# Optimization experiments

Measured on AMD Instinct MI355X. Metric: run time of the kernel, lower is better.

Reference implementation:

```python
import jax, jax.numpy as jnp
import numpy as np

MARGIN = 0.3


def setup_inputs() -> dict:
    key = jax.random.key(0)
    k1, k2 = jax.random.split(key)
    embeddings = jax.random.normal(k1, (4096, 128), dtype=jnp.float32)
    labels = jax.random.randint(k2, (4096,), 0, 256, dtype=jnp.int64)
    return {"embeddings": embeddings, "labels": labels}


def reference(embeddings, labels):
    # L2-normalize rows (same as F.normalize(p=2, dim=1), eps=1e-12)
    norm = jnp.maximum(jnp.linalg.norm(embeddings, axis=1, keepdims=True), 1e-12)
    e = embeddings / norm
    # cosine distance matrix [N, N]
    dist = 1.0 - e @ e.T

    same = labels[None, :] == labels[:, None]          # [N, N]
    n = labels.shape[0]
    eye = jnp.eye(n, dtype=bool)
    pos_mask = same & ~eye                             # positives excl. self
    neg_mask = ~same

    # dist in [0, 2]; finite sentinels keep max/min well-defined per row
    hardest_pos = jnp.max(jnp.where(pos_mask, dist, -1.0), axis=1)
    hardest_neg = jnp.min(jnp.where(neg_mask, dist, 3.0), axis=1)

    valid = jnp.any(pos_mask, axis=1) & jnp.any(neg_mask, axis=1)
    per_row = jax.nn.relu(hardest_pos - hardest_neg + MARGIN)
    loss_sum = jnp.sum(jnp.where(valid, per_row, 0.0))
    count = jnp.sum(valid)
    return loss_sum / jnp.maximum(count, 1).astype(loss_sum.dtype)
```

## Files before the change

kernel.cpp:

```cpp
#include <hip/hip_runtime.h>
#include <stdint.h>

typedef __bf16 bf16x8 __attribute__((ext_vector_type(8)));
typedef float f32x4 __attribute__((ext_vector_type(4)));

#define N_ROWS 4096
#define KD 128
#define BM 128
#define NCHUNK 32
#define CHUNK 128
#define NBLOCKS (32 * NCHUNK)
#define FIN_BLOCKS 64

__device__ __forceinline__ unsigned short f32_to_bf16_rne(float f) {
    union { float f; uint32_t u; } v; v.f = f;
    uint32_t u = v.u;
    return (unsigned short)((u + 0x7FFFu + ((u >> 16) & 1u)) >> 16);
}

__device__ __forceinline__ int swz(int row, int c) { return row * 16 + (c ^ (row & 15)); }
__device__ __forceinline__ int swzL(int L) { return (L & ~15) | ((L & 15) ^ ((L >> 4) & 15)); }

__global__ __launch_bounds__(256) void normalize_kernel(const float* __restrict__ E,
                                                        unsigned short* __restrict__ out,
                                                        unsigned* __restrict__ ctrl) {
    if (blockIdx.x == 0 && threadIdx.x < 3) ctrl[threadIdx.x] = 0u;
    const int wave = threadIdx.x >> 6;
    const int lane = threadIdx.x & 63;
    const int row = blockIdx.x * 4 + wave;
    const float2 v = *(const float2*)&E[row * KD + lane * 2];
    float s = v.x * v.x + v.y * v.y;
#pragma unroll
    for (int m = 1; m < 64; m <<= 1) s += __shfl_xor(s, m, 64);
    float inv = 0.0f;
    if (s > 0.0f) {
        inv = rsqrtf(s);
        inv = inv * (1.5f - 0.5f * s * inv * inv);
    }
    const unsigned short a = f32_to_bf16_rne(v.x * inv);
    const unsigned short b = f32_to_bf16_rne(v.y * inv);
    ((uint32_t*)out)[row * (KD / 2) + lane] = ((uint32_t)b << 16) | a;
}

__global__ __launch_bounds__(256, 4) void gram_kernel(const unsigned short* __restrict__ Ebits,
                                                      const int* __restrict__ labels,
                                                      float2* __restrict__ partials) {
    __shared__ uint4 Bs4[CHUNK * (KD / 8)];
    __shared__ int ljs[CHUNK];

    const int tid = threadIdx.x;
    const int itile = blockIdx.x & 31;
    const int chunk = blockIdx.x >> 5;
    const int ibase = itile * BM;
    const int cbase = chunk * CHUNK;

    const int wave = tid >> 6, lane = tid & 63;
    const int quad = lane >> 4, l15 = lane & 15;

    {
        const uint4* src = (const uint4*)(Ebits + (size_t)cbase * KD);
#pragma unroll
        for (int it = 0; it < 8; ++it) {
            const int Ld = it * 256 + wave * 64 + lane;
            const int Ls = swzL(Ld);
            __builtin_amdgcn_global_load_lds(
                (const __attribute__((address_space(1))) void*)&src[Ls],
                (__attribute__((address_space(3))) void*)&Bs4[it * 256 + wave * 64],
                16, 0, 0);
        }
    }
    if (tid < CHUNK) ljs[tid] = labels[cbase + tid];

    bf16x8 afrag[2][4];
    {
        const uint4* asrc = (const uint4*)Ebits;
#pragma unroll
        for (int mb = 0; mb < 2; ++mb) {
            const int arow = ibase + wave * 32 + mb * 16 + l15;
#pragma unroll
            for (int s = 0; s < 4; ++s)
                afrag[mb][s] = *(const bf16x8*)&asrc[arow * 16 + s * 4 + quad];
        }
    }
    int li_lab[2][4];
#pragma unroll
    for (int mb = 0; mb < 2; ++mb)
#pragma unroll
        for (int r = 0; r < 4; ++r)
            li_lab[mb][r] = labels[ibase + wave * 32 + mb * 16 + quad * 4 + r];

    __syncthreads();

    float minpos[2][4] = {{2.f, 2.f, 2.f, 2.f}, {2.f, 2.f, 2.f, 2.f}};
    float maxneg[2][4] = {{-2.f, -2.f, -2.f, -2.f}, {-2.f, -2.f, -2.f, -2.f}};

#pragma unroll
    for (int t = 0; t < 8; ++t) {
        f32x4 acc0 = {0.f, 0.f, 0.f, 0.f};
        f32x4 acc1 = {0.f, 0.f, 0.f, 0.f};
#pragma unroll
        for (int s = 0; s < 4; ++s) {
            const bf16x8 bfrag = *(const bf16x8*)&Bs4[swz(t * 16 + l15, s * 4 + quad)];
            acc0 = __builtin_amdgcn_mfma_f32_16x16x32_bf16(afrag[0][s], bfrag, acc0, 0, 0, 0);
            acc1 = __builtin_amdgcn_mfma_f32_16x16x32_bf16(afrag[1][s], bfrag, acc1, 0, 0, 0);
        }
        const int jg = cbase + t * 16 + l15;
        const int lj = ljs[t * 16 + l15];
#pragma unroll
        for (int mb = 0; mb < 2; ++mb) {
            const int ig0 = ibase + wave * 32 + mb * 16 + quad * 4;
#pragma unroll
            for (int r = 0; r < 4; ++r) {
                const float d = (mb == 0) ? acc0[r] : acc1[r];
                const bool same = (lj == li_lab[mb][r]);
                const float dp = (same && (ig0 + r != jg)) ? d : 2.0f;
                const float dn = same ? -2.0f : d;
                minpos[mb][r] = fminf(minpos[mb][r], dp);
                maxneg[mb][r] = fmaxf(maxneg[mb][r], dn);
            }
        }
    }

#pragma unroll
    for (int m = 1; m < 16; m <<= 1) {
#pragma unroll
        for (int mb = 0; mb < 2; ++mb)
#pragma unroll
            for (int r = 0; r < 4; ++r) {
                minpos[mb][r] = fminf(minpos[mb][r], __shfl_xor(minpos[mb][r], m, 64));
                maxneg[mb][r] = fmaxf(maxneg[mb][r], __shfl_xor(maxneg[mb][r], m, 64));
            }
    }
    if (l15 == 0) {
#pragma unroll
        for (int mb = 0; mb < 2; ++mb) {
            const int ig0 = ibase + wave * 32 + mb * 16 + quad * 4;
#pragma unroll
            for (int r = 0; r < 4; ++r)
                partials[(ig0 + r) * NCHUNK + chunk] = make_float2(minpos[mb][r], maxneg[mb][r]);
        }
    }
}

__global__ __launch_bounds__(256) void finalize_kernel(const float2* __restrict__ partials,
                                                       float* __restrict__ gsum,
                                                       unsigned* __restrict__ gcnt,
                                                       unsigned* __restrict__ ticket,
                                                       float* __restrict__ out) {
    __shared__ float ssum[4];
    __shared__ int scnt[4];
    __shared__ unsigned s_old;

    const int tid = threadIdx.x;
    const int sub = tid & 3;
    const int row = blockIdx.x * 64 + (tid >> 2);

    const float4* p4 = (const float4*)&partials[row * NCHUNK];
    float mp = 2.f, mn = -2.f;
#pragma unroll
    for (int k = 0; k < 4; ++k) {
        const float4 v = p4[sub * 4 + k];
        mp = fminf(mp, fminf(v.x, v.z));
        mn = fmaxf(mn, fmaxf(v.y, v.w));
    }
    mp = fminf(mp, __shfl_xor(mp, 1, 64)); mp = fminf(mp, __shfl_xor(mp, 2, 64));
    mn = fmaxf(mn, __shfl_xor(mn, 1, 64)); mn = fmaxf(mn, __shfl_xor(mn, 2, 64));

    float sum = 0.f; int cnt = 0;
    if (sub == 0 && mp < 1.5f && mn > -1.5f) {
        sum = fmaxf(0.f, mn - mp + 0.3f);
        cnt = 1;
    }
#pragma unroll
    for (int m = 1; m < 64; m <<= 1) {
        sum += __shfl_xor(sum, m, 64);
        cnt += __shfl_xor(cnt, m, 64);
    }
    const int wave = tid >> 6, lane = tid & 63;
    if (lane == 0) { ssum[wave] = sum; scnt[wave] = cnt; }
    __syncthreads();
    if (tid == 0) {
        atomicAdd(gsum, ssum[0] + ssum[1] + ssum[2] + ssum[3]);
        atomicAdd(gcnt, (unsigned)(scnt[0] + scnt[1] + scnt[2] + scnt[3]));
    }
    __syncthreads();
    if (tid == 0) s_old = atomicAdd(ticket, 1u);
    __syncthreads();
    if (s_old == (unsigned)(FIN_BLOCKS - 1) && tid == 0) {
        const float S = __hip_atomic_load(gsum, __ATOMIC_RELAXED, __HIP_MEMORY_SCOPE_AGENT);
        const unsigned C = __hip_atomic_load(gcnt, __ATOMIC_RELAXED, __HIP_MEMORY_SCOPE_AGENT);
        out[0] = S / (float)(C > 0u ? C : 1u);
    }
}

extern "C" void kernel_launch(void* const* d_in, const int* in_sizes, int n_in,
                              void* d_out, int out_size, void* d_ws, size_t ws_size,
                              hipStream_t stream) {
    const float* E = (const float*)d_in[0];
    const int* labels = (const int*)d_in[1];

    unsigned short* ebits = (unsigned short*)d_ws;
    float2* partials = (float2*)((char*)d_ws + (size_t)N_ROWS * KD * 2);
    unsigned* ctrl = (unsigned*)(partials + N_ROWS * NCHUNK);
    float* gsum = (float*)&ctrl[0];
    unsigned* gcnt = &ctrl[1];
    unsigned* ticket = &ctrl[2];
    float* out = (float*)d_out;

    normalize_kernel<<<N_ROWS / 4, 256, 0, stream>>>(E, ebits, ctrl);
    gram_kernel<<<NBLOCKS, 256, 0, stream>>>(ebits, labels, partials);
    finalize_kernel<<<FIN_BLOCKS, 256, 0, stream>>>(partials, gsum, gcnt, ticket, out);
}
```

Before: 72.27 us.

## Fuse normalize, gram and finalize into one kernel with per-tile completion counters

Merges the three kernels into a single launch. Each block normalizes its own A and B row chunks straight into LDS, redoing the normalization for every tile instead of reading a precomputed bf16 copy. The last block to finish each row tile, detected with an atomic counter, reduces that tile's partials, and a second counter picks the block that writes the final loss. This removes two kernel launches and the global bf16 round trip, but adds redundant normalization work and float reads per block, halves the occupancy hint, and adds a memset for the control words.

```diff
diff --git a/kernel.cpp b/kernel.cpp
--- a/kernel.cpp
+++ b/kernel.cpp
@@ -7,10 +7,12 @@
 #define N_ROWS 4096
 #define KD 128
 #define BM 128
+#define CHUNK 128
 #define NCHUNK 32
-#define CHUNK 128
-#define NBLOCKS (32 * NCHUNK)
-#define FIN_BLOCKS 64
+#define NITILE 32
+#define NBLOCKS (NITILE * NCHUNK)
+
+#define CTRL_WORDS 35
 
 __device__ __forceinline__ unsigned short f32_to_bf16_rne(float f) {
     union { float f; uint32_t u; } v; v.f = f;
@@ -19,69 +21,48 @@
 }
 
 __device__ __forceinline__ int swz(int row, int c) { return row * 16 + (c ^ (row & 15)); }
-__device__ __forceinline__ int swzL(int L) { return (L & ~15) | ((L & 15) ^ ((L >> 4) & 15)); }
-
-__global__ __launch_bounds__(256) void normalize_kernel(const float* __restrict__ E,
-                                                        unsigned short* __restrict__ out,
-                                                        unsigned* __restrict__ ctrl) {
-    if (blockIdx.x == 0 && threadIdx.x < 3) ctrl[threadIdx.x] = 0u;
-    const int wave = threadIdx.x >> 6;
-    const int lane = threadIdx.x & 63;
-    const int row = blockIdx.x * 4 + wave;
-    const float2 v = *(const float2*)&E[row * KD + lane * 2];
-    float s = v.x * v.x + v.y * v.y;
-#pragma unroll
-    for (int m = 1; m < 64; m <<= 1) s += __shfl_xor(s, m, 64);
-    float inv = 0.0f;
-    if (s > 0.0f) {
-        inv = rsqrtf(s);
-        inv = inv * (1.5f - 0.5f * s * inv * inv);
-    }
-    const unsigned short a = f32_to_bf16_rne(v.x * inv);
-    const unsigned short b = f32_to_bf16_rne(v.y * inv);
-    ((uint32_t*)out)[row * (KD / 2) + lane] = ((uint32_t)b << 16) | a;
-}
-
-__global__ __launch_bounds__(256, 4) void gram_kernel(const unsigned short* __restrict__ Ebits,
-                                                      const int* __restrict__ labels,
-                                                      float2* __restrict__ partials) {
-    __shared__ uint4 Bs4[CHUNK * (KD / 8)];
-    __shared__ int ljs[CHUNK];
+
+__device__ __forceinline__ void norm_chunk_to_lds(const float* __restrict__ E,
+                                                  unsigned* lds, int gbase,
+                                                  int wave, int lane) {
+#pragma unroll 4
+    for (int rr = 0; rr < 32; ++rr) {
+        const int r = wave * 32 + rr;
+        const float2 v = *(const float2*)&E[(size_t)(gbase + r) * KD + lane * 2];
+        float s = v.x * v.x + v.y * v.y;
+#pragma unroll
+        for (int m = 1; m < 64; m <<= 1) s += __shfl_xor(s, m, 64);
+        float inv = 0.0f;
+        if (s > 0.0f) {
+            inv = rsqrtf(s);
+            inv = inv * (1.5f - 0.5f * s * inv * inv);
+        }
+        const unsigned short a = f32_to_bf16_rne(v.x * inv);
+        const unsigned short b = f32_to_bf16_rne(v.y * inv);
+        lds[swz(r, lane >> 2) * 4 + (lane & 3)] = ((unsigned)b << 16) | a;
+    }
+}
+
+__global__ __launch_bounds__(256, 2) void fused_kernel(const float* __restrict__ E,
+                                                       const int* __restrict__ labels,
+                                                       unsigned long long* __restrict__ partials,
+                                                       unsigned* __restrict__ ctrl,
+                                                       float* __restrict__ out) {
+    __shared__ uint4 AB[4096];
+    uint4* const As4 = AB;
+    uint4* const Bs4 = AB + 2048;
 
     const int tid = threadIdx.x;
     const int itile = blockIdx.x & 31;
     const int chunk = blockIdx.x >> 5;
     const int ibase = itile * BM;
     const int cbase = chunk * CHUNK;
-
     const int wave = tid >> 6, lane = tid & 63;
     const int quad = lane >> 4, l15 = lane & 15;
 
-    {
-        const uint4* src = (const uint4*)(Ebits + (size_t)cbase * KD);
-#pragma unroll
-        for (int it = 0; it < 8; ++it) {
-            const int Ld = it * 256 + wave * 64 + lane;
-            const int Ls = swzL(Ld);
-            __builtin_amdgcn_global_load_lds(
-                (const __attribute__((address_space(1))) void*)&src[Ls],
-                (__attribute__((address_space(3))) void*)&Bs4[it * 256 + wave * 64],
-                16, 0, 0);
-        }
-    }
-    if (tid < CHUNK) ljs[tid] = labels[cbase + tid];
-
-    bf16x8 afrag[2][4];
-    {
-        const uint4* asrc = (const uint4*)Ebits;
-#pragma unroll
-        for (int mb = 0; mb < 2; ++mb) {
-            const int arow = ibase + wave * 32 + mb * 16 + l15;
-#pragma unroll
-            for (int s = 0; s < 4; ++s)
-                afrag[mb][s] = *(const bf16x8*)&asrc[arow * 16 + s * 4 + quad];
-        }
-    }
+    int lj_t[8];
+#pragma unroll
+    for (int t = 0; t < 8; ++t) lj_t[t] = labels[cbase + t * 16 + l15];
     int li_lab[2][4];
 #pragma unroll
     for (int mb = 0; mb < 2; ++mb)
@@ -89,7 +70,20 @@
         for (int r = 0; r < 4; ++r)
             li_lab[mb][r] = labels[ibase + wave * 32 + mb * 16 + quad * 4 + r];
 
-    __syncthreads();
+    norm_chunk_to_lds(E, (unsigned*)Bs4, cbase, wave, lane);
+    const uint4* aLds = Bs4;
+    if (itile != chunk) {
+        norm_chunk_to_lds(E, (unsigned*)As4, ibase, wave, lane);
+        aLds = As4;
+    }
+    __syncthreads();
+
+    bf16x8 afrag[2][4];
+#pragma unroll
+    for (int mb = 0; mb < 2; ++mb)
+#pragma unroll
+        for (int s = 0; s < 4; ++s)
+            afrag[mb][s] = *(const bf16x8*)&aLds[swz(wave * 32 + mb * 16 + l15, s * 4 + quad)];
 
     float minpos[2][4] = {{2.f, 2.f, 2.f, 2.f}, {2.f, 2.f, 2.f, 2.f}};
     float maxneg[2][4] = {{-2.f, -2.f, -2.f, -2.f}, {-2.f, -2.f, -2.f, -2.f}};
@@ -105,7 +99,7 @@
             acc1 = __builtin_amdgcn_mfma_f32_16x16x32_bf16(afrag[1][s], bfrag, acc1, 0, 0, 0);
         }
         const int jg = cbase + t * 16 + l15;
-        const int lj = ljs[t * 16 + l15];
+        const int lj = lj_t[t];
 #pragma unroll
         for (int mb = 0; mb < 2; ++mb) {
             const int ig0 = ibase + wave * 32 + mb * 16 + quad * 4;
@@ -131,43 +125,50 @@
                 maxneg[mb][r] = fmaxf(maxneg[mb][r], __shfl_xor(maxneg[mb][r], m, 64));
             }
     }
+
     if (l15 == 0) {
 #pragma unroll
         for (int mb = 0; mb < 2; ++mb) {
             const int ig0 = ibase + wave * 32 + mb * 16 + quad * 4;
 #pragma unroll
-            for (int r = 0; r < 4; ++r)
-                partials[(ig0 + r) * NCHUNK + chunk] = make_float2(minpos[mb][r], maxneg[mb][r]);
-        }
-    }
-}
-
-__global__ __launch_bounds__(256) void finalize_kernel(const float2* __restrict__ partials,
-                                                       float* __restrict__ gsum,
-                                                       unsigned* __restrict__ gcnt,
-                                                       unsigned* __restrict__ ticket,
-                                                       float* __restrict__ out) {
-    __shared__ float ssum[4];
-    __shared__ int scnt[4];
-    __shared__ unsigned s_old;
-
-    const int tid = threadIdx.x;
-    const int sub = tid & 3;
-    const int row = blockIdx.x * 64 + (tid >> 2);
-
-    const float4* p4 = (const float4*)&partials[row * NCHUNK];
+            for (int r = 0; r < 4; ++r) {
+                union { float2 f; unsigned long long u; } v;
+                v.f = make_float2(minpos[mb][r], maxneg[mb][r]);
+                __hip_atomic_store(&partials[(size_t)(ig0 + r) * NCHUNK + chunk], v.u,
+                                   __ATOMIC_RELAXED, __HIP_MEMORY_SCOPE_AGENT);
+            }
+        }
+    }
+
+    __shared__ unsigned s_flag;
+    __syncthreads();
+    if (tid == 0) {
+        const unsigned o = __hip_atomic_fetch_add(&ctrl[itile], 1u,
+                                                  __ATOMIC_RELAXED, __HIP_MEMORY_SCOPE_AGENT);
+        s_flag = (o == NCHUNK - 1) ? 1u : 0u;
+    }
+    __syncthreads();
+    if (s_flag == 0u) return;
+
+    float* ssum = (float*)AB;
+    int* scnt = (int*)AB + 4;
+    const int row_l = tid >> 1;
+    const int half = tid & 1;
+    const size_t prow = (size_t)(ibase + row_l) * NCHUNK;
     float mp = 2.f, mn = -2.f;
 #pragma unroll
-    for (int k = 0; k < 4; ++k) {
-        const float4 v = p4[sub * 4 + k];
-        mp = fminf(mp, fminf(v.x, v.z));
-        mn = fmaxf(mn, fmaxf(v.y, v.w));
-    }
-    mp = fminf(mp, __shfl_xor(mp, 1, 64)); mp = fminf(mp, __shfl_xor(mp, 2, 64));
-    mn = fmaxf(mn, __shfl_xor(mn, 1, 64)); mn = fmaxf(mn, __shfl_xor(mn, 2, 64));
+    for (int k = 0; k < 16; ++k) {
+        union { float2 f; unsigned long long u; } v;
+        v.u = __hip_atomic_load(&partials[prow + half * 16 + k],
+                                __ATOMIC_RELAXED, __HIP_MEMORY_SCOPE_AGENT);
+        mp = fminf(mp, v.f.x);
+        mn = fmaxf(mn, v.f.y);
+    }
+    mp = fminf(mp, __shfl_xor(mp, 1, 64));
+    mn = fmaxf(mn, __shfl_xor(mn, 1, 64));
 
     float sum = 0.f; int cnt = 0;
-    if (sub == 0 && mp < 1.5f && mn > -1.5f) {
+    if (half == 0 && mp < 1.5f && mn > -1.5f) {
         sum = fmaxf(0.f, mn - mp + 0.3f);
         cnt = 1;
     }
@@ -176,19 +177,22 @@
         sum += __shfl_xor(sum, m, 64);
         cnt += __shfl_xor(cnt, m, 64);
     }
-    const int wave = tid >> 6, lane = tid & 63;
     if (lane == 0) { ssum[wave] = sum; scnt[wave] = cnt; }
     __syncthreads();
     if (tid == 0) {
-        atomicAdd(gsum, ssum[0] + ssum[1] + ssum[2] + ssum[3]);
-        atomicAdd(gcnt, (unsigned)(scnt[0] + scnt[1] + scnt[2] + scnt[3]));
-    }
-    __syncthreads();
-    if (tid == 0) s_old = atomicAdd(ticket, 1u);
-    __syncthreads();
-    if (s_old == (unsigned)(FIN_BLOCKS - 1) && tid == 0) {
-        const float S = __hip_atomic_load(gsum, __ATOMIC_RELAXED, __HIP_MEMORY_SCOPE_AGENT);
-        const unsigned C = __hip_atomic_load(gcnt, __ATOMIC_RELAXED, __HIP_MEMORY_SCOPE_AGENT);
+        atomicAdd((float*)&ctrl[33], ssum[0] + ssum[1] + ssum[2] + ssum[3]);
+        atomicAdd(&ctrl[34], (unsigned)(scnt[0] + scnt[1] + scnt[2] + scnt[3]));
+        asm volatile("s_waitcnt vmcnt(0)" ::: "memory");
+        const unsigned o2 = __hip_atomic_fetch_add(&ctrl[32], 1u,
+                                                   __ATOMIC_RELAXED, __HIP_MEMORY_SCOPE_AGENT);
+        s_flag = (o2 == NITILE - 1) ? 2u : 0u;
+    }
+    __syncthreads();
+    if (s_flag == 2u && tid == 0) {
+        const float S = __hip_atomic_load((float*)&ctrl[33],
+                                          __ATOMIC_RELAXED, __HIP_MEMORY_SCOPE_AGENT);
+        const unsigned C = __hip_atomic_load(&ctrl[34],
+                                             __ATOMIC_RELAXED, __HIP_MEMORY_SCOPE_AGENT);
         out[0] = S / (float)(C > 0u ? C : 1u);
     }
 }
@@ -199,15 +203,10 @@
     const float* E = (const float*)d_in[0];
     const int* labels = (const int*)d_in[1];
 
-    unsigned short* ebits = (unsigned short*)d_ws;
-    float2* partials = (float2*)((char*)d_ws + (size_t)N_ROWS * KD * 2);
-    unsigned* ctrl = (unsigned*)(partials + N_ROWS * NCHUNK);
-    float* gsum = (float*)&ctrl[0];
-    unsigned* gcnt = &ctrl[1];
-    unsigned* ticket = &ctrl[2];
+    unsigned long long* partials = (unsigned long long*)d_ws;
+    unsigned* ctrl = (unsigned*)((char*)d_ws + (size_t)N_ROWS * NCHUNK * 8);
     float* out = (float*)d_out;
 
-    normalize_kernel<<<N_ROWS / 4, 256, 0, stream>>>(E, ebits, ctrl);
-    gram_kernel<<<NBLOCKS, 256, 0, stream>>>(ebits, labels, partials);
-    finalize_kernel<<<FIN_BLOCKS, 256, 0, stream>>>(partials, gsum, gcnt, ticket, out);
-}
+    hipMemsetAsync(ctrl, 0, CTRL_WORDS * sizeof(unsigned), stream);
+    fused_kernel<<<NBLOCKS, 256, 0, stream>>>(E, labels, partials, ctrl, out);
+}
```

Result: slower. 126.8 us (+75.4%).
